# Optimization experiments

Measured on AMD Instinct MI355X. Metric: run time of the kernel, lower is better.

## Reference

```python
import jax, jax.numpy as jnp
import numpy as np

B, T, H, L = 8, 256, 64, 3
NB, NF, HP = 17, 68, 6
K = 9  # temporal kernel
PAD = (K - 1) // 2
EPS = 1e-5


def _normalize(adj):
    adj = adj + np.eye(adj.shape[0], dtype=np.float32)
    d = adj.sum(1)
    dinv = np.power(d, -0.5)
    dinv[np.isinf(dinv)] = 0.0
    return (dinv[:, None] * adj * dinv[None, :]).astype(np.float32)


def _body_adj():
    a = np.zeros((NB, NB), np.float32)
    conns = [(0, 1), (0, 2), (1, 3), (2, 4), (0, 5), (0, 6), (5, 6), (5, 7), (7, 9), (6, 8), (8, 10), (5, 11), (6, 12), (11, 12), (11, 13), (13, 15), (12, 14), (14, 16)]
    for i, j in conns:
        a[i, j] = 1.0
        a[j, i] = 1.0
    return _normalize(a)


def _face_adj():
    a = np.zeros((NF, NF), np.float32)
    for i in range(16): a[i, i + 1] = 1.0
    for i in range(17, 21): a[i, i + 1] = 1.0
    for i in range(22, 26): a[i, i + 1] = 1.0
    for i in range(27, 30): a[i, i + 1] = 1.0
    for i in range(31, 35): a[i, i + 1] = 1.0
    for i in range(36, 41): a[i, i + 1] = 1.0
    a[41, 36] = 1.0
    for i in range(42, 47): a[i, i + 1] = 1.0
    a[47, 42] = 1.0
    for i in range(48, 59): a[i, i + 1] = 1.0
    a[59, 48] = 1.0
    for i in range(60, 67): a[i, i + 1] = 1.0
    a[67, 60] = 1.0
    a = a + a.T
    return _normalize(a)


def setup_inputs() -> dict:
    keys = iter(jax.random.split(jax.random.key(0), 80))

    def rn(shape, s):
        return jax.random.normal(next(keys), shape, jnp.float32) * s

    inp = {}
    inp['body_kps'] = jax.random.normal(next(keys), (B, T, NB * 2), jnp.float32)
    inp['face_kps_2d'] = jax.random.normal(next(keys), (B, T, NF * 2), jnp.float32)
    inp['head_pose'] = jax.random.normal(next(keys), (B, T, HP), jnp.float32)
    inp['body_adj'] = jnp.asarray(_body_adj())
    inp['face_adj'] = jnp.asarray(_face_adj())
    inp['body_proj_w'] = rn((2, H), 0.5)
    inp['body_proj_b'] = jnp.zeros((H,), jnp.float32)
    inp['face_proj_w'] = rn((2, H), 0.5)
    inp['face_proj_b'] = jnp.zeros((H,), jnp.float32)
    inp['head_w'] = rn((HP, H), 0.3)
    inp['head_b'] = jnp.zeros((H,), jnp.float32)
    for p in ('b', 'f'):
        inp[p + '_t1w'] = rn((L, H, H, K), 0.04)
        inp[p + '_t1b'] = jnp.zeros((L, H), jnp.float32)
        inp[p + '_bn1g'] = jnp.ones((L, H), jnp.float32)
        inp[p + '_bn1b'] = jnp.zeros((L, H), jnp.float32)
        inp[p + '_bn1m'] = rn((L, H), 0.1)
        inp[p + '_bn1v'] = jax.random.uniform(next(keys), (L, H), jnp.float32, 0.5, 1.5)
        inp[p + '_gcw'] = rn((L, H, H), 0.1)
        inp[p + '_gcb'] = jnp.zeros((L, H), jnp.float32)
        inp[p + '_t2w'] = rn((L, H, H, K), 0.04)
        inp[p + '_t2b'] = jnp.zeros((L, H), jnp.float32)
        inp[p + '_bn2g'] = jnp.ones((L, H), jnp.float32)
        inp[p + '_bn2b'] = jnp.zeros((L, H), jnp.float32)
        inp[p + '_bn2m'] = rn((L, H), 0.1)
        inp[p + '_bn2v'] = jax.random.uniform(next(keys), (L, H), jnp.float32, 0.5, 1.5)
    total = NB * H + NF * H + H  # 5504
    inp['fus1_w'] = rn((total, 4 * H), 0.02)
    inp['fus1_b'] = jnp.zeros((4 * H,), jnp.float32)
    inp['fus2_w'] = rn((4 * H, 2 * H), 0.06)
    inp['fus2_b'] = jnp.zeros((2 * H,), jnp.float32)
    inp['fus3_w'] = rn((2 * H, H), 0.09)
    inp['fus3_b'] = jnp.zeros((H,), jnp.float32)
    inp['fus4_w'] = rn((H, 5), 0.12)
    inp['fus4_b'] = jnp.zeros((5,), jnp.float32)
    return inp


def _conv_bn(x, w, b, g, be, m, v):
    # x: (BN, C, T); w: (O, I, K). Conv1d (pad=4) + eval-mode BatchNorm1d.
    y = jax.lax.conv_general_dilated(x, w, (1,), [(PAD, PAD)], dimension_numbers=('NCH', 'OIH', 'NCH'))
    y = y + b[None, :, None]
    inv = g * jax.lax.rsqrt(v + EPS)
    return y * inv[None, :, None] + (be - m * inv)[None, :, None]


def _block(x, adj, t1w, t1b, g1, b1, m1, v1, gw, gb, t2w, t2b, g2, b2, m2, v2):
    # x: (B, N, C, T); residual is identity (in_channels == out_channels)
    Bn, N, C, Tn = x.shape
    res = x
    h = jax.nn.relu(_conv_bn(x.reshape(Bn * N, C, Tn), t1w, t1b, g1, b1, m1, v1)).reshape(Bn, N, C, Tn)
    # spatial graph conv, batched over all timesteps at once (adj @ (x W) + b)
    support = jnp.einsum('bnct,co->bnot', h, gw)
    h = jax.nn.relu(jnp.einsum('mn,bnot->bmot', adj, support) + gb[None, None, :, None])
    h = _conv_bn(h.reshape(Bn * N, C, Tn), t2w, t2b, g2, b2, m2, v2).reshape(Bn, N, C, Tn)
    return h + res  # dropout = identity in eval


def _stream(x, n_nodes, pw, pb, adj, ps):
    Bn, Tn, _ = x.shape
    h = x.reshape(Bn, Tn, n_nodes, 2) @ pw + pb          # (B, T, N, H)
    h = jnp.transpose(h, (0, 2, 3, 1))                   # (B, N, H, T)
    for l in range(ps[0].shape[0]):
        h = _block(h, adj, *(p[l] for p in ps))
    return h.mean(axis=3).reshape(Bn, -1)                # temporal mean-pool, flatten nodes


def reference(body_kps, face_kps_2d, head_pose, body_adj, face_adj, body_proj_w, body_proj_b, face_proj_w, face_proj_b, head_w, head_b, b_t1w, b_t1b, b_bn1g, b_bn1b, b_bn1m, b_bn1v, b_gcw, b_gcb, b_t2w, b_t2b, b_bn2g, b_bn2b, b_bn2m, b_bn2v, f_t1w, f_t1b, f_bn1g, f_bn1b, f_bn1m, f_bn1v, f_gcw, f_gcb, f_t2w, f_t2b, f_bn2g, f_bn2b, f_bn2m, f_bn2v, fus1_w, fus1_b, fus2_w, fus2_b, fus3_w, fus3_b, fus4_w, fus4_b):
    bps = (b_t1w, b_t1b, b_bn1g, b_bn1b, b_bn1m, b_bn1v, b_gcw, b_gcb, b_t2w, b_t2b, b_bn2g, b_bn2b, b_bn2m, b_bn2v)
    fps = (f_t1w, f_t1b, f_bn1g, f_bn1b, f_bn1m, f_bn1v, f_gcw, f_gcb, f_t2w, f_t2b, f_bn2g, f_bn2b, f_bn2m, f_bn2v)
    bf = _stream(body_kps, NB, body_proj_w, body_proj_b, body_adj, bps)
    ff = _stream(face_kps_2d, NF, face_proj_w, face_proj_b, face_adj, fps)
    hp = jax.nn.relu(head_pose @ head_w + head_b).mean(axis=1)
    feat = jnp.concatenate([bf, ff, hp], axis=-1)
    h = jax.nn.relu(feat @ fus1_w + fus1_b)
    h = jax.nn.relu(h @ fus2_w + fus2_b)
    h = jax.nn.relu(h @ fus3_w + fus3_b)
    return h @ fus4_w + fus4_b
```

## Files before the change

### kernel.cpp

```cpp
#include <hip/hip_runtime.h>

constexpr int B_ = 8, T_ = 256, H_ = 64, L_ = 3, NB_ = 17, NF_ = 68, HP_ = 6, K_ = 9;
constexpr int FEAT_DIM = NB_ * H_ + NF_ * H_ + H_;
constexpr int HT = H_ * T_;

typedef _Float16 half4_t __attribute__((ext_vector_type(4)));
typedef _Float16 half8_t __attribute__((ext_vector_type(8)));
typedef float f32x16 __attribute__((ext_vector_type(16)));
typedef float f32x4 __attribute__((ext_vector_type(4)));

constexpr size_t SZ_AB = (size_t)B_ * NB_ * HT;
constexpr size_t SZ_AF = (size_t)B_ * NF_ * HT;
constexpr size_t OFF_TB   = 0;
constexpr size_t OFF_TF   = OFF_TB + SZ_AB / 2;
constexpr size_t OFF_SUPB = OFF_TF + SZ_AF / 2;
constexpr size_t OFF_SUPF = OFF_SUPB + SZ_AB / 2;
constexpr size_t OFF_GB   = OFF_SUPF + SZ_AF / 2;
constexpr size_t OFF_GF   = OFF_GB + SZ_AB / 2;
constexpr size_t OFF_W3   = OFF_GF + SZ_AF / 2;
constexpr size_t OFF_GW3  = OFF_W3 + 4 * 55296;
constexpr size_t OFF_B2   = OFF_GW3 + 2 * 6144;
constexpr size_t OFF_ADJPB= OFF_B2 + 768;
constexpr size_t OFF_ADJPF= OFF_ADJPB + 512;
constexpr size_t OFF_FEAT = OFF_ADJPF + 3840;
constexpr size_t OFF_P1   = OFF_FEAT + (size_t)B_ * FEAT_DIM;

struct ConvPrepSet { const float *w, *tb, *g, *bb, *m, *v; };

struct Args {
    const float *body_kps, *face_kps, *head_pose, *body_adj, *face_adj;
    const float *body_pw, *body_pb, *face_pw, *face_pb, *head_w, *head_b;
    ConvPrepSet sb1, sb2, sf1, sf2;
    const float *b_gcw, *f_gcw, *b_gcb, *f_gcb;
    const float *fus1_w, *fus1_b, *fus2_w, *fus2_b, *fus3_w, *fus3_b, *fus4_w, *fus4_b;
    _Float16 *TrB, *TrF, *SupB, *SupF, *Gb, *Gf;
    _Float16 *W3, *GW3, *adjPB, *adjPF;
    float *B2, *p1, *feat;
    float *out;
};

__device__ __forceinline__ half8_t ld_b8(const _Float16* p) {
    half4_t lo = *(const half4_t*)p;
    half4_t hi = *(const half4_t*)(p + 4);
    return __builtin_shufflevector(lo, hi, 0, 1, 2, 3, 4, 5, 6, 7);
}

__device__ __forceinline__ void st_b8(_Float16* p, half8_t v) {
    half4_t lo, hi;
#pragma unroll
    for (int j = 0; j < 4; ++j) { lo[j] = v[j]; hi[j] = v[4 + j]; }
    *(half4_t*)p = lo;
    *(half4_t*)(p + 4) = hi;
}

__device__ __forceinline__ void stage_chunk64(const _Float16* __restrict__ xb,
                                              _Float16* __restrict__ Xs, int tc, int tid) {
    for (int u = tid; u < 72 * 8; u += 256) {
        int row = u >> 3, c = u & 7;
        int t = tc * 64 + row - 4;
        half8_t v;
        if (t >= 0 && t < T_) {
            v = *(const half8_t*)(xb + (size_t)t * H_ + c * 8);
        } else {
#pragma unroll
            for (int j = 0; j < 8; ++j) v[j] = (_Float16)0.f;
        }
        st_b8(&Xs[row * 68 + c * 8], v);
    }
}

__device__ __forceinline__ void stage_res64(const _Float16* __restrict__ xb,
                                            _Float16* __restrict__ Rs, int tc, int tid) {
    for (int u = tid; u < 64 * 8; u += 256) {
        int row = u >> 3, c = u & 7;
        half8_t v = *(const half8_t*)(xb + (size_t)(tc * 64 + row) * H_ + c * 8);
        st_b8(&Rs[row * 68 + c * 8], v);
    }
}

__device__ __forceinline__ void conv_kloop(const half8_t* __restrict__ wl,
                                           const _Float16* __restrict__ Xs,
                                           int trow, int ln31, int kg, int ot,
                                           f32x16& acc) {
    const _Float16* xr0 = Xs + (size_t)(trow + ln31) * 68;
#pragma unroll
    for (int tap = 0; tap < K_; ++tap) {
#pragma unroll
        for (int ks = 0; ks < 4; ++ks) {
            int i8 = ks * 2 + kg;
            half8_t a = wl[(tap * 8 + i8) * H_ + ot * 32 + ln31];
            half8_t bf = ld_b8(xr0 + tap * 68 + i8 * 8);
            acc = __builtin_amdgcn_mfma_f32_32x32x16_f16(a, bf, acc, 0, 0, 0);
        }
    }
}

__device__ void convmix_core(const half8_t* __restrict__ wl,
                             const float* __restrict__ b1l,
                             const half8_t* __restrict__ gl,
                             _Float16* __restrict__ supb,
                             int tc, _Float16* __restrict__ Xs, int tid) {
    int ln = tid & 63;
    int w = __builtin_amdgcn_readfirstlane(tid >> 6);
    int ln31 = ln & 31, kg = ln >> 5;
    int ts = w & 1, ot = w >> 1;
    int trow = ts * 32;

    f32x16 acc;
#pragma unroll
    for (int r = 0; r < 16; ++r) acc[r] = 0.f;

    conv_kloop(wl, Xs, trow, ln31, kg, ot, acc);
    __syncthreads();

    _Float16* mrow = Xs + (size_t)(4 + trow + ln31) * 68;
#pragma unroll
    for (int rg = 0; rg < 4; ++rg) {
        int o0 = ot * 32 + rg * 8 + kg * 4;
        f32x4 bv = *(const f32x4*)(b1l + o0);
        half4_t hv;
#pragma unroll
        for (int j = 0; j < 4; ++j)
            hv[j] = (_Float16)fmaxf(acc[rg * 4 + j] + bv[j], 0.f);
        *(half4_t*)(mrow + o0) = hv;
    }
    __syncthreads();

    f32x16 acc2;
#pragma unroll
    for (int r = 0; r < 16; ++r) acc2[r] = 0.f;
#pragma unroll
    for (int ks = 0; ks < 4; ++ks) {
        int i8 = ks * 2 + kg;
        half8_t a = gl[i8 * H_ + ot * 32 + ln31];
        half8_t bf = ld_b8(mrow + i8 * 8);
        acc2 = __builtin_amdgcn_mfma_f32_32x32x16_f16(a, bf, acc2, 0, 0, 0);
    }
    __syncthreads();

#pragma unroll
    for (int rg = 0; rg < 4; ++rg) {
        int o0 = ot * 32 + rg * 8 + kg * 4;
        half4_t hv;
#pragma unroll
        for (int j = 0; j < 4; ++j)
            hv[j] = (_Float16)acc2[rg * 4 + j];
        *(half4_t*)(mrow + o0) = hv;
    }
    __syncthreads();
    _Float16* gout = supb + (size_t)(tc * 64) * H_;
    const _Float16* srow = Xs + 4 * 68;
#pragma unroll
    for (int k2 = 0; k2 < 2; ++k2) {
        int u = k2 * 256 + tid;
        int r = u >> 3, c = u & 7;
        half8_t v = ld_b8(srow + r * 68 + c * 8);
        *(half8_t*)(gout + (size_t)r * H_ + c * 8) = v;
    }
}

__global__ __launch_bounds__(256) void prep_k(Args A) {
    int blk = blockIdx.x;
    int tid = threadIdx.x;
    if (blk < 1728) {
        int set = blk / 432;
        int bx = blk % 432;
        ConvPrepSet s = (set == 0) ? A.sb1 : (set == 1) ? A.sb2 : (set == 2) ? A.sf1 : A.sf2;
        int idx = bx * 256 + tid;
        int k = idx % K_; int r = idx / K_;
        int i = r % H_; r /= H_;
        int o = r % H_; int l = r / H_;
        float sc = s.g[l * H_ + o] * rsqrtf(s.v[l * H_ + o] + 1e-5f);
        A.W3[(size_t)set * 110592 + ((((l * K_ + k) * 8 + (i >> 3)) * H_ + o) * 8) + (i & 7)]
            = (_Float16)(s.w[idx] * sc);
        if (i == 0 && k == 0)
            A.B2[set * 192 + l * H_ + o] =
                s.tb[l * H_ + o] * sc + s.bb[l * H_ + o] - s.m[l * H_ + o] * sc;
    } else if (blk < 1824) {
        int set = (blk - 1728) / 48;
        int bx = (blk - 1728) % 48;
        const float* gw = set ? A.f_gcw : A.b_gcw;
        int idx = bx * 256 + tid;
        int o = idx % H_; int r = idx / H_;
        int c = r % H_; int l = r / H_;
        A.GW3[(size_t)set * 12288 + (((l * 8 + (c >> 3)) * H_ + o) * 8) + (c & 7)]
            = (_Float16)gw[idx];
    } else {
        int idx = (blk - 1824) * 256 + tid;
        if (idx < 1024) {
            int m = idx >> 5, k = idx & 31;
            A.adjPB[idx] = (m < NB_ && k < NB_) ? (_Float16)A.body_adj[m * NB_ + k] : (_Float16)0.f;
        } else if (idx < 8704) {
            int j = idx - 1024;
            int m = j / 80, k = j % 80;
            A.adjPF[j] = (m < NF_ && k < NF_) ? (_Float16)A.face_adj[m * NF_ + k] : (_Float16)0.f;
        } else if (idx < 10752) {
            A.p1[idx - 8704] = 0.f;
        } else if (idx < 10752 + B_ * FEAT_DIM) {
            A.feat[idx - 10752] = 0.f;
        }
    }
}

__global__ __launch_bounds__(256, 8) void projcm_k(Args A) {
    __shared__ __align__(16) _Float16 Xs[72 * 68];
    int blk = blockIdx.x, tid = threadIdx.x;
    bool isB = blk < 4 * B_ * NB_;
    int j = isB ? blk : blk - 4 * B_ * NB_;
    int bn = j >> 2, tc = j & 3;
    const float* kps = isB ? A.body_kps : A.face_kps;
    const float* pw  = isB ? A.body_pw  : A.face_pw;
    const float* pb  = isB ? A.body_pb  : A.face_pb;
    _Float16* trunk  = isB ? A.TrB : A.TrF;
    int N = isB ? NB_ : NF_;
    int b = bn / N, n = bn % N;

    if (tid < 144) {
        int row = tid >> 1, hf = tid & 1;
        int t = tc * 64 + row - 4;
        _Float16* xr = Xs + row * 68 + hf * 32;
        if (t >= 0 && t < T_) {
            float x0 = kps[((size_t)b * T_ + t) * (N * 2) + n * 2 + 0];
            float x1 = kps[((size_t)b * T_ + t) * (N * 2) + n * 2 + 1];
            bool own = (row >= 4 && row < 68);
            _Float16* ob = trunk + (size_t)bn * HT + (size_t)t * H_ + hf * 32;
#pragma unroll
            for (int cg2 = 0; cg2 < 4; ++cg2) {
                half8_t v;
#pragma unroll
                for (int jj = 0; jj < 8; ++jj) {
                    int c = hf * 32 + cg2 * 8 + jj;
                    v[jj] = (_Float16)fmaf(x0, pw[c], fmaf(x1, pw[H_ + c], pb[c]));
                }
                st_b8(xr + cg2 * 8, v);
                if (own) *(half8_t*)(ob + cg2 * 8) = v;
            }
        } else {
            half8_t z;
#pragma unroll
            for (int jj = 0; jj < 8; ++jj) z[jj] = (_Float16)0.f;
            st_b8(xr, z);
            st_b8(xr + 8, z);
            st_b8(xr + 16, z);
            st_b8(xr + 24, z);
        }
    }
    __syncthreads();

    const half8_t* w1 = (const half8_t*)(A.W3 + (isB ? 0 : 221184));
    const float* b1l  = isB ? A.B2 : A.B2 + 384;
    const half8_t* gl = (const half8_t*)(A.GW3 + (isB ? 0 : 12288));
    _Float16* supb = (isB ? A.SupB : A.SupF) + (size_t)bn * HT;
    convmix_core(w1, b1l, gl, supb, tc, Xs, tid);
}

__global__ __launch_bounds__(256, 8) void cm_k(Args A, int l) {
    __shared__ __align__(16) _Float16 Xs[72 * 68];
    int blk = blockIdx.x, tid = threadIdx.x;
    bool isB = blk < 4 * B_ * NB_;
    int j = isB ? blk : blk - 4 * B_ * NB_;
    int bn = j >> 2, tc = j & 3;
    const _Float16* trunk = isB ? A.TrB : A.TrF;

    stage_chunk64(trunk + (size_t)bn * HT, Xs, tc, tid);
    __syncthreads();

    const half8_t* w1 = (const half8_t*)(A.W3 + (isB ? 0 : 221184)) + (size_t)l * (K_ * 8 * H_);
    const float* b1l  = (isB ? A.B2 : A.B2 + 384) + l * H_;
    const half8_t* gl = (const half8_t*)(A.GW3 + (isB ? 0 : 12288)) + (size_t)l * (8 * H_);
    _Float16* supb = (isB ? A.SupB : A.SupF) + (size_t)bn * HT;
    convmix_core(w1, b1l, gl, supb, tc, Xs, tid);
}

template <int N, int MT, int KS>
__device__ void adjmix_impl(const _Float16* __restrict__ sup,
                            const half8_t* __restrict__ adjP,
                            const float* __restrict__ gb,
                            _Float16* __restrict__ out,
                            int blk, int l, _Float16* Ls, int tid) {
    constexpr int KP = KS * 16;
    constexpr int PITCH = KP + 4;
    int b = blk >> 7, cb = blk & 127;
    int colbase = cb * 128;

    for (int u = tid; u < KP * 16; u += 256) {
        int n = u >> 4, cs = u & 15;
        half8_t v;
        if (n < N) v = *(const half8_t*)(sup + (size_t)(b * N + n) * HT + colbase + cs * 8);
        else {
#pragma unroll
            for (int j = 0; j < 8; ++j) v[j] = (_Float16)0.f;
        }
#pragma unroll
        for (int j = 0; j < 8; ++j) Ls[(cs * 8 + j) * PITCH + n] = v[j];
    }
    __syncthreads();

    int ln = tid & 63;
    int w = __builtin_amdgcn_readfirstlane(tid >> 6);
    int ln31 = ln & 31, kg = ln >> 5;
    int colL = w * 32 + ln31;

    f32x16 acc[MT];
#pragma unroll
    for (int mt = 0; mt < MT; ++mt)
#pragma unroll
        for (int r = 0; r < 16; ++r) acc[mt][r] = 0.f;

#pragma unroll
    for (int ks = 0; ks < KS; ++ks) {
        half8_t bf = ld_b8(&Ls[colL * PITCH + ks * 16 + kg * 8]);
#pragma unroll
        for (int mt = 0; mt < MT; ++mt) {
            half8_t af = adjP[(size_t)(mt * 32 + ln31) * (KP / 8) + ks * 2 + kg];
            acc[mt] = __builtin_amdgcn_mfma_f32_32x32x16_f16(af, bf, acc[mt], 0, 0, 0);
        }
    }
    __syncthreads();

    float gbv = gb[l * H_ + (colL & 63)];
#pragma unroll
    for (int mt = 0; mt < MT; ++mt) {
#pragma unroll
        for (int r = 0; r < 16; ++r) {
            int m = mt * 32 + (r & 3) + 8 * (r >> 2) + 4 * kg;
            Ls[m * 132 + colL] = (_Float16)fmaxf(acc[mt][r] + gbv, 0.f);
        }
    }
    __syncthreads();

    for (int u = tid; u < N * 16; u += 256) {
        int m = u >> 4, c = u & 15;
        half8_t v = ld_b8(&Ls[m * 132 + c * 8]);
        *(half8_t*)(out + (size_t)(b * N + m) * HT + colbase + c * 8) = v;
    }
}

__global__ __launch_bounds__(256) void adjmix_k(Args A, int l) {
    __shared__ __align__(16) _Float16 Ls[12800];
    int blk = blockIdx.x, tid = threadIdx.x;
    if (blk < 1024)
        adjmix_impl<NB_, 1, 2>(A.SupB, (const half8_t*)A.adjPB, A.b_gcb, A.Gb, blk, l, Ls, tid);
    else
        adjmix_impl<NF_, 3, 5>(A.SupF, (const half8_t*)A.adjPF, A.f_gcb, A.Gf, blk - 1024, l, Ls, tid);
}

__global__ __launch_bounds__(256, 8) void c2_k(Args A, int l) {
    __shared__ __align__(16) _Float16 Xs[72 * 68];
    __shared__ __align__(16) _Float16 Rs[64 * 68];
    int blk = blockIdx.x, tid = threadIdx.x;
    bool isB = blk < 4 * B_ * NB_;
    int j = isB ? blk : blk - 4 * B_ * NB_;
    int bn = j >> 2, tc = j & 3;
    const _Float16* G = isB ? A.Gb : A.Gf;
    _Float16* trunk   = isB ? A.TrB : A.TrF;
    const half8_t* w2 = (const half8_t*)(A.W3 + (isB ? 110592 : 331776)) + (size_t)l * (K_ * 8 * H_);
    const float* b2l  = (isB ? A.B2 + 192 : A.B2 + 576) + l * H_;

    stage_chunk64(G + (size_t)bn * HT, Xs, tc, tid);
    stage_res64(trunk + (size_t)bn * HT, Rs, tc, tid);
    __syncthreads();

    int ln = tid & 63;
    int w = __builtin_amdgcn_readfirstlane(tid >> 6);
    int ln31 = ln & 31, kg = ln >> 5;
    int ts = w & 1, ot = w >> 1;
    int trow = ts * 32;

    f32x16 acc;
#pragma unroll
    for (int r = 0; r < 16; ++r) acc[r] = 0.f;

    conv_kloop(w2, Xs, trow, ln31, kg, ot, acc);
    __syncthreads();

    {
        _Float16* orow = Xs + (size_t)(4 + trow + ln31) * 68;
        const _Float16* rrow = Rs + (size_t)(trow + ln31) * 68;
#pragma unroll
        for (int rg = 0; rg < 4; ++rg) {
            int o0 = ot * 32 + rg * 8 + kg * 4;
            f32x4 bv = *(const f32x4*)(b2l + o0);
            half4_t rv = *(const half4_t*)(rrow + o0);
            half4_t hv;
#pragma unroll
            for (int jj = 0; jj < 4; ++jj)
                hv[jj] = (_Float16)(acc[rg * 4 + jj] + bv[jj] + (float)rv[jj]);
            *(half4_t*)(orow + o0) = hv;
        }
    }
    __syncthreads();

    _Float16* gout = trunk + (size_t)bn * HT + (size_t)(tc * 64) * H_;
    const _Float16* srow = Xs + 4 * 68;
#pragma unroll
    for (int k2 = 0; k2 < 2; ++k2) {
        int u = k2 * 256 + tid;
        int r = u >> 3, c = u & 7;
        half8_t v = ld_b8(srow + r * 68 + c * 8);
        *(half8_t*)(gout + (size_t)r * H_ + c * 8) = v;
    }
}

__global__ __launch_bounds__(256, 8) void c2last_k(Args A) {
    __shared__ __align__(16) _Float16 Xs[72 * 68];
    __shared__ __align__(16) _Float16 Rs[64 * 68];
    int blk = blockIdx.x, tid = threadIdx.x;
    if (blk >= 2720) {
        int b = blk - 2720;
        if (tid < 64) {
            int c = tid;
            float w0 = A.head_w[c], w1 = A.head_w[64 + c], w2 = A.head_w[128 + c],
                  w3 = A.head_w[192 + c], w4 = A.head_w[256 + c], w5 = A.head_w[320 + c];
            float bias = A.head_b[c];
            float acc = 0.f;
            for (int t = 0; t < T_; ++t) {
                const float* xr = A.head_pose + ((size_t)b * T_ + t) * HP_;
                float s = fmaf(xr[0], w0, fmaf(xr[1], w1, fmaf(xr[2], w2,
                          fmaf(xr[3], w3, fmaf(xr[4], w4, fmaf(xr[5], w5, bias))))));
                acc += fmaxf(s, 0.f);
            }
            A.feat[(size_t)b * FEAT_DIM + NB_ * H_ + NF_ * H_ + c] = acc * (1.f / 256.f);
        }
        return;
    }
    constexpr int l = L_ - 1;
    bool isB = blk < 4 * B_ * NB_;
    int j = isB ? blk : blk - 4 * B_ * NB_;
    int bn = j >> 2, tc = j & 3;
    const _Float16* G = isB ? A.Gb : A.Gf;
    _Float16* trunk   = isB ? A.TrB : A.TrF;
    const half8_t* w2 = (const half8_t*)(A.W3 + (isB ? 110592 : 331776)) + (size_t)l * (K_ * 8 * H_);
    const float* b2l  = (isB ? A.B2 + 192 : A.B2 + 576) + l * H_;
    int N = isB ? NB_ : NF_;
    int fbase = isB ? 0 : NB_ * H_;

    stage_chunk64(G + (size_t)bn * HT, Xs, tc, tid);
    stage_res64(trunk + (size_t)bn * HT, Rs, tc, tid);
    __syncthreads();

    int ln = tid & 63;
    int w = __builtin_amdgcn_readfirstlane(tid >> 6);
    int ln31 = ln & 31, kg = ln >> 5;
    int ts = w & 1, ot = w >> 1;
    int trow = ts * 32;

    f32x16 acc;
#pragma unroll
    for (int r = 0; r < 16; ++r) acc[r] = 0.f;

    conv_kloop(w2, Xs, trow, ln31, kg, ot, acc);

    float sv[16];
    const _Float16* rrow = Rs + (size_t)(trow + ln31) * 68;
#pragma unroll
    for (int rg = 0; rg < 4; ++rg) {
        int o0 = ot * 32 + rg * 8 + kg * 4;
        f32x4 bv = *(const f32x4*)(b2l + o0);
        half4_t rv = *(const half4_t*)(rrow + o0);
#pragma unroll
        for (int jj = 0; jj < 4; ++jj) {
            int r = rg * 4 + jj;
            float s = acc[r] + bv[jj] + (float)rv[jj];
#pragma unroll
            for (int off = 1; off < 32; off <<= 1) s += __shfl_xor(s, off);
            sv[r] = s;
        }
    }
    __syncthreads();
    float* red = (float*)Xs;
    if (ln31 == 0) {
#pragma unroll
        for (int r = 0; r < 16; ++r) {
            int olocal = (r & 3) + 8 * (r >> 2) + 4 * kg;
            red[w * 32 + olocal] = sv[r];
        }
    }
    __syncthreads();
    if (tid < 64) {
        int o = tid, ot2 = o >> 5, ol = o & 31;
        float s = red[(ot2 * 2) * 32 + ol] + red[(ot2 * 2 + 1) * 32 + ol];
        int b = bn / N, n = bn % N;
        atomicAdd(&A.feat[(size_t)b * FEAT_DIM + fbase + n * H_ + o], s * (1.f / 256.f));
    }
}

__global__ __launch_bounds__(256) void fus1_k(Args A) {
    __shared__ float fv[8][64];
    int blk = blockIdx.x;
    int ic = blk >> 1, kh = blk & 1;
    int base = ic * 128 + kh * 64;
    int tid = threadIdx.x;
    for (int u = tid; u < 8 * 64; u += 256) {
        int b = u >> 6, j = u & 63;
        fv[b][j] = A.feat[(size_t)b * FEAT_DIM + base + j];
    }
    __syncthreads();
    float acc[8];
#pragma unroll
    for (int b = 0; b < 8; ++b) acc[b] = 0.f;
    const float* wb = A.fus1_w + (size_t)base * 256 + tid;
    for (int i = 0; i < 64; ++i) {
        float wv = wb[(size_t)i * 256];
#pragma unroll
        for (int b = 0; b < 8; ++b) acc[b] = fmaf(fv[b][i], wv, acc[b]);
    }
#pragma unroll
    for (int b = 0; b < 8; ++b) atomicAdd(&A.p1[b * 256 + tid], acc[b]);
}

__global__ __launch_bounds__(256) void fus_tail_k(Args A) {
    __shared__ float s1[256], s2[128], s3[64];
    int b = blockIdx.x, tid = threadIdx.x;
    s1[tid] = fmaxf(A.p1[b * 256 + tid] + A.fus1_b[tid], 0.f);
    __syncthreads();
    if (tid < 128) {
        float acc = A.fus2_b[tid];
        for (int i = 0; i < 256; ++i) acc = fmaf(s1[i], A.fus2_w[i * 128 + tid], acc);
        s2[tid] = fmaxf(acc, 0.f);
    }
    __syncthreads();
    if (tid < 64) {
        float acc = A.fus3_b[tid];
        for (int i = 0; i < 128; ++i) acc = fmaf(s2[i], A.fus3_w[i * 64 + tid], acc);
        s3[tid] = fmaxf(acc, 0.f);
    }
    __syncthreads();
    if (tid < 5) {
        float acc = A.fus4_b[tid];
        for (int i = 0; i < 64; ++i) acc = fmaf(s3[i], A.fus4_w[i * 5 + tid], acc);
        A.out[b * 5 + tid] = acc;
    }
}

extern "C" void kernel_launch(void* const* d_in, const int* in_sizes, int n_in,
                              void* d_out, int out_size, void* d_ws, size_t ws_size,
                              hipStream_t stream) {
    float* ws = (float*)d_ws;

    Args A;
    A.body_kps = (const float*)d_in[0];
    A.face_kps = (const float*)d_in[1];
    A.head_pose = (const float*)d_in[2];
    A.body_adj = (const float*)d_in[3];
    A.face_adj = (const float*)d_in[4];
    A.body_pw = (const float*)d_in[5];
    A.body_pb = (const float*)d_in[6];
    A.face_pw = (const float*)d_in[7];
    A.face_pb = (const float*)d_in[8];
    A.head_w = (const float*)d_in[9];
    A.head_b = (const float*)d_in[10];
    A.sb1 = ConvPrepSet{(const float*)d_in[11], (const float*)d_in[12], (const float*)d_in[13],
                        (const float*)d_in[14], (const float*)d_in[15], (const float*)d_in[16]};
    A.b_gcw = (const float*)d_in[17];
    A.b_gcb = (const float*)d_in[18];
    A.sb2 = ConvPrepSet{(const float*)d_in[19], (const float*)d_in[20], (const float*)d_in[21],
                        (const float*)d_in[22], (const float*)d_in[23], (const float*)d_in[24]};
    A.sf1 = ConvPrepSet{(const float*)d_in[25], (const float*)d_in[26], (const float*)d_in[27],
                        (const float*)d_in[28], (const float*)d_in[29], (const float*)d_in[30]};
    A.f_gcw = (const float*)d_in[31];
    A.f_gcb = (const float*)d_in[32];
    A.sf2 = ConvPrepSet{(const float*)d_in[33], (const float*)d_in[34], (const float*)d_in[35],
                        (const float*)d_in[36], (const float*)d_in[37], (const float*)d_in[38]};
    A.fus1_w = (const float*)d_in[39]; A.fus1_b = (const float*)d_in[40];
    A.fus2_w = (const float*)d_in[41]; A.fus2_b = (const float*)d_in[42];
    A.fus3_w = (const float*)d_in[43]; A.fus3_b = (const float*)d_in[44];
    A.fus4_w = (const float*)d_in[45]; A.fus4_b = (const float*)d_in[46];

    A.TrB  = (_Float16*)(ws + OFF_TB);
    A.TrF  = (_Float16*)(ws + OFF_TF);
    A.SupB = (_Float16*)(ws + OFF_SUPB);
    A.SupF = (_Float16*)(ws + OFF_SUPF);
    A.Gb   = (_Float16*)(ws + OFF_GB);
    A.Gf   = (_Float16*)(ws + OFF_GF);
    A.W3   = (_Float16*)(ws + OFF_W3);
    A.GW3  = (_Float16*)(ws + OFF_GW3);
    A.adjPB= (_Float16*)(ws + OFF_ADJPB);
    A.adjPF= (_Float16*)(ws + OFF_ADJPF);
    A.B2   = ws + OFF_B2;
    A.feat = ws + OFF_FEAT;
    A.p1   = ws + OFF_P1;
    A.out  = (float*)d_out;

    const int gconv = 4 * (B_ * NB_ + B_ * NF_);

    prep_k<<<2038, 256, 0, stream>>>(A);
    projcm_k<<<gconv, 256, 0, stream>>>(A);
    for (int l = 0; l < L_; ++l) {
        adjmix_k<<<2048, 256, 0, stream>>>(A, l);
        if (l < L_ - 1) {
            c2_k<<<gconv, 256, 0, stream>>>(A, l);
            cm_k<<<gconv, 256, 0, stream>>>(A, l + 1);
        } else {
            c2last_k<<<gconv + 8, 256, 0, stream>>>(A);
        }
    }
    fus1_k<<<86, 256, 0, stream>>>(A);
    fus_tail_k<<<8, 256, 0, stream>>>(A);
}
```

Before: 372.8 us.

## Process two time chunks per block with register-prefetched double-buffered staging

cm_k and c2_k now give each block two consecutive 64-step time chunks instead of one, halving the grid. While the first chunk's convolution runs, the next chunk's input is loaded into registers and then written to a second LDS buffer. In c2_k the residual is loaded straight from global memory into registers, so the Rs buffer goes away. This aims to hide global load latency behind MFMA work and cut per-block overhead, at the cost of fewer blocks, lower occupancy hints (launch bounds 6) and more register pressure.

```diff
diff --git a/kernel.cpp b/kernel.cpp
--- a/kernel.cpp
+++ b/kernel.cpp
@@ -76,6 +76,47 @@
         half8_t v = *(const half8_t*)(xb + (size_t)(tc * 64 + row) * H_ + c * 8);
         st_b8(&Rs[row * 68 + c * 8], v);
     }
+}
+
+struct SReg { half8_t v[3]; };
+
+__device__ __forceinline__ void issue_stage(const _Float16* __restrict__ xb, int tc, int tid,
+                                            SReg& S) {
+#pragma unroll
+    for (int k = 0; k < 3; ++k) {
+        int u = k * 256 + tid;
+        if (u < 576) {
+            int row = u >> 3, c = u & 7;
+            int t = tc * 64 + row - 4;
+            if (t >= 0 && t < T_) {
+                S.v[k] = *(const half8_t*)(xb + (size_t)t * H_ + c * 8);
+            } else {
+#pragma unroll
+                for (int j = 0; j < 8; ++j) S.v[k][j] = (_Float16)0.f;
+            }
+        }
+    }
+}
+
+__device__ __forceinline__ void write_stage(_Float16* __restrict__ Xs, int tid, const SReg& S) {
+#pragma unroll
+    for (int k = 0; k < 3; ++k) {
+        int u = k * 256 + tid;
+        if (u < 576) {
+            int row = u >> 3, c = u & 7;
+            st_b8(&Xs[row * 68 + c * 8], S.v[k]);
+        }
+    }
+}
+
+struct RReg { half4_t r[4]; };
+
+__device__ __forceinline__ void issue_res(const _Float16* __restrict__ tb, int tc, int trow,
+                                          int ln31, int kg, int ot, RReg& R) {
+    const _Float16* rr = tb + (size_t)(tc * 64 + trow + ln31) * H_ + ot * 32 + kg * 4;
+#pragma unroll
+    for (int rg = 0; rg < 4; ++rg)
+        R.r[rg] = *(const half4_t*)(rr + rg * 8);
 }
 
 __device__ __forceinline__ void conv_kloop(const half8_t* __restrict__ wl,
@@ -254,22 +295,37 @@
     convmix_core(w1, b1l, gl, supb, tc, Xs, tid);
 }
 
-__global__ __launch_bounds__(256, 8) void cm_k(Args A, int l) {
-    __shared__ __align__(16) _Float16 Xs[72 * 68];
+__global__ __launch_bounds__(256, 6) void cm_k(Args A, int l) {
+    __shared__ __align__(16) _Float16 Xs[2][72 * 68];
     int blk = blockIdx.x, tid = threadIdx.x;
-    bool isB = blk < 4 * B_ * NB_;
-    int j = isB ? blk : blk - 4 * B_ * NB_;
-    int bn = j >> 2, tc = j & 3;
-    const _Float16* trunk = isB ? A.TrB : A.TrF;
-
-    stage_chunk64(trunk + (size_t)bn * HT, Xs, tc, tid);
-    __syncthreads();
+    bool isB = blk < 2 * B_ * NB_;
+    int j = isB ? blk : blk - 2 * B_ * NB_;
+    int bn = j >> 1, half = j & 1;
+    const _Float16* trunk = (isB ? A.TrB : A.TrF) + (size_t)bn * HT;
 
     const half8_t* w1 = (const half8_t*)(A.W3 + (isB ? 0 : 221184)) + (size_t)l * (K_ * 8 * H_);
     const float* b1l  = (isB ? A.B2 : A.B2 + 384) + l * H_;
     const half8_t* gl = (const half8_t*)(A.GW3 + (isB ? 0 : 12288)) + (size_t)l * (8 * H_);
     _Float16* supb = (isB ? A.SupB : A.SupF) + (size_t)bn * HT;
-    convmix_core(w1, b1l, gl, supb, tc, Xs, tid);
+
+    {
+        SReg S;
+        issue_stage(trunk, half * 2, tid, S);
+        write_stage(Xs[0], tid, S);
+    }
+    __syncthreads();
+
+#pragma unroll 1
+    for (int i = 0; i < 2; ++i) {
+        int tc = half * 2 + i;
+        SReg Sn;
+        if (i == 0) issue_stage(trunk, tc + 1, tid, Sn);
+        convmix_core(w1, b1l, gl, supb, tc, Xs[i], tid);
+        if (i == 0) {
+            write_stage(Xs[1], tid, Sn);
+            __syncthreads();
+        }
+    }
 }
 
 template <int N, int MT, int KS>
@@ -345,21 +401,16 @@
         adjmix_impl<NF_, 3, 5>(A.SupF, (const half8_t*)A.adjPF, A.f_gcb, A.Gf, blk - 1024, l, Ls, tid);
 }
 
-__global__ __launch_bounds__(256, 8) void c2_k(Args A, int l) {
-    __shared__ __align__(16) _Float16 Xs[72 * 68];
-    __shared__ __align__(16) _Float16 Rs[64 * 68];
+__global__ __launch_bounds__(256, 6) void c2_k(Args A, int l) {
+    __shared__ __align__(16) _Float16 Xs[2][72 * 68];
     int blk = blockIdx.x, tid = threadIdx.x;
-    bool isB = blk < 4 * B_ * NB_;
-    int j = isB ? blk : blk - 4 * B_ * NB_;
-    int bn = j >> 2, tc = j & 3;
-    const _Float16* G = isB ? A.Gb : A.Gf;
-    _Float16* trunk   = isB ? A.TrB : A.TrF;
+    bool isB = blk < 2 * B_ * NB_;
+    int j = isB ? blk : blk - 2 * B_ * NB_;
+    int bn = j >> 1, half = j & 1;
+    const _Float16* G = (isB ? A.Gb : A.Gf) + (size_t)bn * HT;
+    _Float16* trunk   = (isB ? A.TrB : A.TrF) + (size_t)bn * HT;
     const half8_t* w2 = (const half8_t*)(A.W3 + (isB ? 110592 : 331776)) + (size_t)l * (K_ * 8 * H_);
     const float* b2l  = (isB ? A.B2 + 192 : A.B2 + 576) + l * H_;
-
-    stage_chunk64(G + (size_t)bn * HT, Xs, tc, tid);
-    stage_res64(trunk + (size_t)bn * HT, Rs, tc, tid);
-    __syncthreads();
 
     int ln = tid & 63;
     int w = __builtin_amdgcn_readfirstlane(tid >> 6);
@@ -367,38 +418,55 @@
     int ts = w & 1, ot = w >> 1;
     int trow = ts * 32;
 
-    f32x16 acc;
-#pragma unroll
-    for (int r = 0; r < 16; ++r) acc[r] = 0.f;
-
-    conv_kloop(w2, Xs, trow, ln31, kg, ot, acc);
-    __syncthreads();
-
     {
-        _Float16* orow = Xs + (size_t)(4 + trow + ln31) * 68;
-        const _Float16* rrow = Rs + (size_t)(trow + ln31) * 68;
-#pragma unroll
-        for (int rg = 0; rg < 4; ++rg) {
-            int o0 = ot * 32 + rg * 8 + kg * 4;
-            f32x4 bv = *(const f32x4*)(b2l + o0);
-            half4_t rv = *(const half4_t*)(rrow + o0);
-            half4_t hv;
-#pragma unroll
-            for (int jj = 0; jj < 4; ++jj)
-                hv[jj] = (_Float16)(acc[rg * 4 + jj] + bv[jj] + (float)rv[jj]);
-            *(half4_t*)(orow + o0) = hv;
-        }
-    }
-    __syncthreads();
-
-    _Float16* gout = trunk + (size_t)bn * HT + (size_t)(tc * 64) * H_;
-    const _Float16* srow = Xs + 4 * 68;
-#pragma unroll
-    for (int k2 = 0; k2 < 2; ++k2) {
-        int u = k2 * 256 + tid;
-        int r = u >> 3, c = u & 7;
-        half8_t v = ld_b8(srow + r * 68 + c * 8);
-        *(half8_t*)(gout + (size_t)r * H_ + c * 8) = v;
+        SReg S;
+        issue_stage(G, half * 2, tid, S);
+        write_stage(Xs[0], tid, S);
+    }
+    __syncthreads();
+
+#pragma unroll 1
+    for (int i = 0; i < 2; ++i) {
+        int tc = half * 2 + i;
+        RReg R;
+        issue_res(trunk, tc, trow, ln31, kg, ot, R);
+        SReg Sn;
+        if (i == 0) issue_stage(G, tc + 1, tid, Sn);
+
+        f32x16 acc;
+#pragma unroll
+        for (int r = 0; r < 16; ++r) acc[r] = 0.f;
+        conv_kloop(w2, Xs[i], trow, ln31, kg, ot, acc);
+
+        if (i == 0) write_stage(Xs[1], tid, Sn);
+        __syncthreads();
+
+        {
+            _Float16* orow = Xs[i] + (size_t)(4 + trow + ln31) * 68;
+#pragma unroll
+            for (int rg = 0; rg < 4; ++rg) {
+                int o0 = ot * 32 + rg * 8 + kg * 4;
+                f32x4 bv = *(const f32x4*)(b2l + o0);
+                half4_t rv = R.r[rg];
+                half4_t hv;
+#pragma unroll
+                for (int jj = 0; jj < 4; ++jj)
+                    hv[jj] = (_Float16)(acc[rg * 4 + jj] + bv[jj] + (float)rv[jj]);
+                *(half4_t*)(orow + o0) = hv;
+            }
+        }
+        __syncthreads();
+
+        _Float16* gout = trunk + (size_t)(tc * 64) * H_;
+        const _Float16* srow = Xs[i] + 4 * 68;
+#pragma unroll
+        for (int k2 = 0; k2 < 2; ++k2) {
+            int u2 = k2 * 256 + tid;
+            int r = u2 >> 3, c = u2 & 7;
+            half8_t v = ld_b8(srow + r * 68 + c * 8);
+            *(half8_t*)(gout + (size_t)r * H_ + c * 8) = v;
+        }
+        if (i == 0) __syncthreads();
     }
 }
 
@@ -583,14 +651,15 @@
     A.out  = (float*)d_out;
 
     const int gconv = 4 * (B_ * NB_ + B_ * NF_);
+    const int gdb   = 2 * (B_ * NB_ + B_ * NF_);
 
     prep_k<<<2038, 256, 0, stream>>>(A);
     projcm_k<<<gconv, 256, 0, stream>>>(A);
     for (int l = 0; l < L_; ++l) {
         adjmix_k<<<2048, 256, 0, stream>>>(A, l);
         if (l < L_ - 1) {
-            c2_k<<<gconv, 256, 0, stream>>>(A, l);
-            cm_k<<<gconv, 256, 0, stream>>>(A, l + 1);
+            c2_k<<<gdb, 256, 0, stream>>>(A, l);
+            cm_k<<<gdb, 256, 0, stream>>>(A, l + 1);
         } else {
             c2last_k<<<gconv + 8, 256, 0, stream>>>(A);
         }
```

New measurement: 501.1 us. +34.4%, slower.
